# Kernel tuning notes

Measured on AMD Instinct MI355X. Metric: run time of the kernel, lower is better.

## Reference

```python
import jax, jax.numpy as jnp
import numpy as np
from jax import lax

DIM = 384
NH = 8
HD = DIM // NH
M = 16          # num_anchors
B = 16
HH = 64
WW = 64
N = HH * WW
STD = 0.02


def setup_inputs() -> dict:
    key = jax.random.key(0)
    ks = jax.random.split(key, 12)
    rn = lambda k, shape: (jax.random.normal(k, shape, jnp.float32) * STD)
    return {
        "x": jax.random.normal(ks[0], (B, N, DIM), jnp.float32),
        "H": HH,
        "W": WW,
        "saliency_w": rn(ks[1], (DIM, 1)),
        "saliency_b": jnp.zeros((1,), jnp.float32),
        "anchor_seeds": rn(ks[2], (1, M, DIM)),
        "w_q_agg": rn(ks[3], (DIM, DIM)),
        "w_kv_agg": rn(ks[4], (DIM, 2 * DIM)),
        "w_q_self": rn(ks[5], (DIM, DIM)),
        "w_kv_self": rn(ks[6], (DIM, 2 * DIM)),
        "w_q_bcast": rn(ks[7], (DIM, DIM)),
        "w_kv_bcast": rn(ks[8], (DIM, 2 * DIM)),
        "dw_kernel": rn(ks[9], (DIM, 1, 3, 3)),  # depthwise conv, OIHW with I=1
        "w_proj": rn(ks[10], (DIM, DIM)),
    }


def _mhsa(q_in, kv_in, wq, wkv):
    """Multi-head cross attention. q_in: [B,Lq,C], kv_in: [B,Lk,C]."""
    b, lq, c = q_in.shape
    lk = kv_in.shape[1]
    scale = HD ** -0.5
    q = (q_in @ wq).reshape(b, lq, NH, HD)
    kv = (kv_in @ wkv).reshape(b, lk, 2, NH, HD)
    k, v = kv[:, :, 0], kv[:, :, 1]
    attn = jnp.einsum("bqhd,bkhd->bhqk", q, k) * scale
    attn = jax.nn.softmax(attn, axis=-1)
    out = jnp.einsum("bhqk,bkhd->bqhd", attn, v).reshape(b, lq, c)
    return out


def reference(x, H, W, saliency_w, saliency_b, anchor_seeds,
              w_q_agg, w_kv_agg, w_q_self, w_kv_self,
              w_q_bcast, w_kv_bcast, dw_kernel, w_proj):
    b, n, c = x.shape
    # saliency gating
    sal = jax.nn.sigmoid(x @ saliency_w + saliency_b)  # [B,N,1]
    x_sal = x * sal
    # stage 1: anchors aggregate from saliency-gated tokens
    anchors = jnp.broadcast_to(anchor_seeds, (b, M, c))
    anchors = anchors + _mhsa(anchors, x_sal, w_q_agg, w_kv_agg)
    # stage 2: anchor self-attention
    anchors = anchors + _mhsa(anchors, anchors, w_q_self, w_kv_self)
    # stage 3: broadcast anchors back to all tokens
    global_out = _mhsa(x, anchors, w_q_bcast, w_kv_bcast)
    # depthwise 3x3 conv on the 2D token map
    x2d = x.reshape(b, H, W, c).transpose(0, 3, 1, 2)  # NCHW
    local = lax.conv_general_dilated(
        x2d, dw_kernel, window_strides=(1, 1), padding="SAME",
        feature_group_count=c,
        dimension_numbers=("NCHW", "OIHW", "NCHW"))
    local = local.transpose(0, 2, 3, 1).reshape(b, n, c)
    return (global_out + local) @ w_proj
```

## Files before the change

### kernel.cpp

```cpp
#include <hip/hip_runtime.h>
#include <hip/hip_bf16.h>

#define SCALE 0.14433756729740643f

typedef __attribute__((ext_vector_type(8))) short bf16x8;
typedef __attribute__((ext_vector_type(4))) float f32x4;

template <typename T> __device__ inline T cvt_from_f(float v);
template <> __device__ inline float cvt_from_f<float>(float v) { return v; }
template <> __device__ inline __hip_bfloat16 cvt_from_f<__hip_bfloat16>(float v) { return __float2bfloat16(v); }

__device__ inline void gload16(const void* g, void* l) {
  __builtin_amdgcn_global_load_lds((const __attribute__((address_space(1))) void*)g,
                                   (__attribute__((address_space(3))) void*)l, 16, 0, 0);
}

__device__ inline int xcd_flat(int nwg) {
  int flat = (blockIdx.z * gridDim.y + blockIdx.y) * gridDim.x + blockIdx.x;
  int per = nwg >> 3;
  return (flat & 7) * per + (flat >> 3);
}

__global__ __launch_bounds__(256) void prep(const float* __restrict__ x,
                                            const float* __restrict__ wsal,
                                            const float* __restrict__ bsal,
                                            __hip_bfloat16* __restrict__ xb,
                                            float* __restrict__ sal) {
  int wave = threadIdx.x >> 6, lane = threadIdx.x & 63;
  size_t row = (size_t)blockIdx.x * 4 + wave;
  const float* xr = x + row * 384;
  float xs[6];
  float part = 0.f;
#pragma unroll
  for (int j = 0; j < 6; j++) {
    int c = lane + 64 * j;
    xs[j] = xr[c];
    part += xs[j] * wsal[c];
  }
#pragma unroll
  for (int off = 32; off >= 1; off >>= 1) part += __shfl_xor(part, off);
  float s = 1.f / (1.f + __expf(-(part + bsal[0])));
#pragma unroll
  for (int j = 0; j < 6; j++) {
    int c = lane + 64 * j;
    xb[row * 384 + c] = __float2bfloat16(xs[j]);
  }
  if (lane == 0) sal[row] = s;
}

__global__ __launch_bounds__(256) void xtrans(const __hip_bfloat16* __restrict__ xb,
                                              __hip_bfloat16* __restrict__ xbT) {
  __shared__ short t[64][66];
  int n0 = blockIdx.x * 64, c0 = blockIdx.y * 64, b = blockIdx.z;
  int tid = threadIdx.x;
  int r = tid >> 3, c8 = tid & 7;
#pragma unroll
  for (int i = 0; i < 2; i++) {
    int row = r + i * 32;
    bf16x8 v = *(const bf16x8*)(xb + ((size_t)(b * 4096 + n0 + row)) * 384 + c0 + c8 * 8);
    unsigned int* trow = (unsigned int*)&t[row][c8 * 8];
#pragma unroll
    for (int j = 0; j < 4; j++) {
      union { unsigned int u; short s[2]; } p;
      p.s[0] = v[j * 2];
      p.s[1] = v[j * 2 + 1];
      trow[j] = p.u;
    }
  }
  __syncthreads();
#pragma unroll
  for (int i = 0; i < 2; i++) {
    int crow = r + i * 32;
    short tb[8];
#pragma unroll
    for (int j = 0; j < 8; j++) tb[j] = t[c8 * 8 + j][crow];
    *(ulonglong2*)(xbT + ((size_t)b * 384 + c0 + crow) * 4096 + n0 + c8 * 8) = *(ulonglong2*)tb;
  }
}

__global__ void wcast_tv(const float* __restrict__ w, __hip_bfloat16* __restrict__ wt) {
  int idx = blockIdx.x * 256 + threadIdx.x;
  if (idx >= 384 * 384) return;
  int n = idx / 384, k = idx % 384;
  wt[idx] = __float2bfloat16(w[(size_t)k * 768 + 384 + n]);
}

template <int K, typename OT, int BSHIFT>
__global__ __launch_bounds__(256) void gemm_mfma(const __hip_bfloat16* __restrict__ A,
                                                 const __hip_bfloat16* __restrict__ BT,
                                                 OT* __restrict__ out, int Ncols,
                                                 size_t btBatchStride) {
  __shared__ __align__(16) __hip_bfloat16 Asl[128][32];
  __shared__ __align__(16) __hip_bfloat16 Bsl[128][32];
  int nf = xcd_flat(gridDim.x * gridDim.y);
  int bX = nf % gridDim.x, bY = nf / gridDim.x;
  int tid = threadIdx.x;
  int lane = tid & 63;
  int w = tid >> 6;
  int wr = w >> 1, wc = w & 1;
  int fr = lane & 15, fq = lane >> 4;
  int rowBase = bY * 128, colBase = bX * 128;
  const __hip_bfloat16* BTb = BT + (size_t)(rowBase >> BSHIFT) * btBatchStride;

  int r1 = tid >> 2, kc1 = tid & 3;
  int r2 = (tid + 256) >> 2;

  char* aB1 = (char*)Asl + (size_t)(w * 64) * 16;
  char* aB2 = (char*)Asl + (size_t)(256 + w * 64) * 16;
  char* bB1 = (char*)Bsl + (size_t)(w * 64) * 16;
  char* bB2 = (char*)Bsl + (size_t)(256 + w * 64) * 16;

  const __hip_bfloat16* a1 = A + (size_t)(rowBase + r1) * K + kc1 * 8;
  const __hip_bfloat16* a2 = A + (size_t)(rowBase + r2) * K + kc1 * 8;
  const __hip_bfloat16* b1 = BTb + (size_t)(colBase + r1) * K + kc1 * 8;
  const __hip_bfloat16* b2 = BTb + (size_t)(colBase + r2) * K + kc1 * 8;

  f32x4 acc[4][4] = {};

  for (int kk = 0; kk < K; kk += 32) {
    gload16(a1 + kk, aB1);
    gload16(a2 + kk, aB2);
    gload16(b1 + kk, bB1);
    gload16(b2 + kk, bB2);
    __syncthreads();
    bf16x8 af[4], bfv[4];
#pragma unroll
    for (int m = 0; m < 4; m++) af[m] = *(const bf16x8*)&Asl[wr * 64 + m * 16 + fr][fq * 8];
#pragma unroll
    for (int n = 0; n < 4; n++) bfv[n] = *(const bf16x8*)&Bsl[wc * 64 + n * 16 + fr][fq * 8];
#pragma unroll
    for (int m = 0; m < 4; m++)
#pragma unroll
      for (int n = 0; n < 4; n++)
        acc[m][n] = __builtin_amdgcn_mfma_f32_16x16x32_bf16(af[m], bfv[n], acc[m][n], 0, 0, 0);
    __syncthreads();
  }

#pragma unroll
  for (int m = 0; m < 4; m++) {
    int row0 = rowBase + wr * 64 + m * 16 + fq * 4;
#pragma unroll
    for (int n = 0; n < 4; n++) {
      int col = colBase + wc * 64 + n * 16 + fr;
      f32x4 v = acc[m][n];
#pragma unroll
      for (int r = 0; r < 4; r++) out[(size_t)(row0 + r) * Ncols + col] = cvt_from_f<OT>(v[r]);
    }
  }
}

__global__ __launch_bounds__(256) void gemm_logits(const __hip_bfloat16* __restrict__ A,
                                                   const __hip_bfloat16* __restrict__ BT,
                                                   __hip_bfloat16* __restrict__ lgT,
                                                   const float* __restrict__ rowScale) {
  constexpr int K = 384;
  __shared__ __align__(16) __hip_bfloat16 Asl[128][32];
  __shared__ __align__(16) __hip_bfloat16 Bsl[128][32];
  int tid = threadIdx.x;
  int lane = tid & 63;
  int w = tid >> 6;
  int wr = w >> 1, wc = w & 1;
  int fr = lane & 15, fq = lane >> 4;
  int rowBase = blockIdx.x * 128;

  int r1 = tid >> 2, kc1 = tid & 3;
  int r2 = (tid + 256) >> 2;

  char* aB1 = (char*)Asl + (size_t)(w * 64) * 16;
  char* aB2 = (char*)Asl + (size_t)(256 + w * 64) * 16;
  char* bB1 = (char*)Bsl + (size_t)(w * 64) * 16;
  char* bB2 = (char*)Bsl + (size_t)(256 + w * 64) * 16;

  const __hip_bfloat16* a1 = A + (size_t)(rowBase + r1) * K + kc1 * 8;
  const __hip_bfloat16* a2 = A + (size_t)(rowBase + r2) * K + kc1 * 8;
  const __hip_bfloat16* b1 = BT + (size_t)r1 * K + kc1 * 8;
  const __hip_bfloat16* b2 = BT + (size_t)r2 * K + kc1 * 8;

  f32x4 acc[4][4] = {};

  for (int kk = 0; kk < K; kk += 32) {
    gload16(a1 + kk, aB1);
    gload16(a2 + kk, aB2);
    gload16(b1 + kk, bB1);
    gload16(b2 + kk, bB2);
    __syncthreads();
    bf16x8 af[4], bfv[4];
#pragma unroll
    for (int m = 0; m < 4; m++) af[m] = *(const bf16x8*)&Asl[wr * 64 + m * 16 + fr][fq * 8];
#pragma unroll
    for (int n = 0; n < 4; n++) bfv[n] = *(const bf16x8*)&Bsl[wc * 64 + n * 16 + fr][fq * 8];
#pragma unroll
    for (int m = 0; m < 4; m++)
#pragma unroll
      for (int n = 0; n < 4; n++)
        acc[m][n] = __builtin_amdgcn_mfma_f32_16x16x32_bf16(af[m], bfv[n], acc[m][n], 0, 0, 0);
    __syncthreads();
  }

  float sv[4][4];
#pragma unroll
  for (int m = 0; m < 4; m++)
#pragma unroll
    for (int r = 0; r < 4; r++)
      sv[m][r] = rowScale[rowBase + wr * 64 + m * 16 + fq * 4 + r];

#pragma unroll
  for (int m = 0; m < 4; m++) {
    int row0 = rowBase + wr * 64 + m * 16 + fq * 4;
    int bb = row0 >> 12;
    int n0 = row0 & 4095;
#pragma unroll
    for (int n = 0; n < 4; n++) {
      int col = wc * 64 + n * 16 + fr;
      __hip_bfloat16 tb[4];
#pragma unroll
      for (int r = 0; r < 4; r++) tb[r] = __float2bfloat16(acc[m][n][r] * sv[m][r]);
      *(unsigned long long*)(lgT + ((size_t)bb * 128 + col) * 4096 + n0) = *(unsigned long long*)tb;
    }
  }
}

__global__ __launch_bounds__(256) void softmax_rows(const __hip_bfloat16* __restrict__ lgT,
                                                    const float* __restrict__ sal,
                                                    __hip_bfloat16* __restrict__ PT) {
  int g = blockIdx.x;
  const __hip_bfloat16* row = lgT + (size_t)g * 4096;
  int tid = threadIdx.x, wv = tid >> 6, lane = tid & 63;
  __shared__ float redm[4], reds[4];
  float v[16];
  union { ulonglong2 u; __hip_bfloat16 h[8]; } L0, L1;
  L0.u = *(const ulonglong2*)(row + tid * 16);
  L1.u = *(const ulonglong2*)(row + tid * 16 + 8);
#pragma unroll
  for (int i = 0; i < 8; i++) {
    v[i] = __bfloat162float(L0.h[i]);
    v[8 + i] = __bfloat162float(L1.h[i]);
  }
  float mx = v[0];
#pragma unroll
  for (int i = 1; i < 16; i++) mx = fmaxf(mx, v[i]);
#pragma unroll
  for (int off = 1; off < 64; off <<= 1) mx = fmaxf(mx, __shfl_xor(mx, off));
  if (lane == 0) redm[wv] = mx;
  __syncthreads();
  mx = fmaxf(fmaxf(redm[0], redm[1]), fmaxf(redm[2], redm[3]));
  float s = 0.f;
#pragma unroll
  for (int i = 0; i < 16; i++) {
    v[i] = __expf(v[i] - mx);
    s += v[i];
  }
#pragma unroll
  for (int off = 1; off < 64; off <<= 1) s += __shfl_xor(s, off);
  if (lane == 0) reds[wv] = s;
  __syncthreads();
  s = (reds[0] + reds[1]) + (reds[2] + reds[3]);
  float inv = 1.f / s;
  const float* sp = sal + (size_t)(g >> 7) * 4096 + tid * 16;
  float salv[16];
#pragma unroll
  for (int i = 0; i < 4; i++) {
    float4 q = *(const float4*)(sp + i * 4);
    salv[i * 4] = q.x; salv[i * 4 + 1] = q.y; salv[i * 4 + 2] = q.z; salv[i * 4 + 3] = q.w;
  }
  __hip_bfloat16 tb[16];
#pragma unroll
  for (int i = 0; i < 16; i++) tb[i] = __float2bfloat16(v[i] * inv * salv[i]);
  __hip_bfloat16* op = PT + (size_t)g * 4096 + tid * 16;
  *(ulonglong2*)op = *(ulonglong2*)tb;
  *(ulonglong2*)(op + 8) = *(ulonglong2*)(tb + 8);
}

__global__ __launch_bounds__(256) void gemm_pvx(const __hip_bfloat16* __restrict__ PT,
                                                const __hip_bfloat16* __restrict__ xbT,
                                                float* __restrict__ pbuf) {
  __shared__ __align__(16) __hip_bfloat16 Asl[128][32];
  __shared__ __align__(16) __hip_bfloat16 Bsl[128][32];
  int nf = xcd_flat(192);
  int bX = nf % 3, bY = (nf / 3) & 15, kz = nf / 48;
  int tid = threadIdx.x;
  int lane = tid & 63;
  int w = tid >> 6;
  int wr = w >> 1, wc = w & 1;
  int fr = lane & 15, fq = lane >> 4;
  int rowBase = bY * 128, colBase = bX * 128;
  const __hip_bfloat16* BTb = xbT + (size_t)bY * 384 * 4096;

  int r1 = tid >> 2, kc1 = tid & 3;
  int r2 = (tid + 256) >> 2;

  char* aB1 = (char*)Asl + (size_t)(w * 64) * 16;
  char* aB2 = (char*)Asl + (size_t)(256 + w * 64) * 16;
  char* bB1 = (char*)Bsl + (size_t)(w * 64) * 16;
  char* bB2 = (char*)Bsl + (size_t)(256 + w * 64) * 16;

  const __hip_bfloat16* a1 = PT + (size_t)(rowBase + r1) * 4096 + kz * 1024 + kc1 * 8;
  const __hip_bfloat16* a2 = PT + (size_t)(rowBase + r2) * 4096 + kz * 1024 + kc1 * 8;
  const __hip_bfloat16* b1 = BTb + (size_t)(colBase + r1) * 4096 + kz * 1024 + kc1 * 8;
  const __hip_bfloat16* b2 = BTb + (size_t)(colBase + r2) * 4096 + kz * 1024 + kc1 * 8;

  f32x4 acc[4][4] = {};

  for (int kk = 0; kk < 1024; kk += 32) {
    gload16(a1 + kk, aB1);
    gload16(a2 + kk, aB2);
    gload16(b1 + kk, bB1);
    gload16(b2 + kk, bB2);
    __syncthreads();
    bf16x8 af[4], bfv[4];
#pragma unroll
    for (int m = 0; m < 4; m++) af[m] = *(const bf16x8*)&Asl[wr * 64 + m * 16 + fr][fq * 8];
#pragma unroll
    for (int n = 0; n < 4; n++) bfv[n] = *(const bf16x8*)&Bsl[wc * 64 + n * 16 + fr][fq * 8];
#pragma unroll
    for (int m = 0; m < 4; m++)
#pragma unroll
      for (int n = 0; n < 4; n++)
        acc[m][n] = __builtin_amdgcn_mfma_f32_16x16x32_bf16(af[m], bfv[n], acc[m][n], 0, 0, 0);
    __syncthreads();
  }

  float* outz = pbuf + (size_t)kz * 786432;
#pragma unroll
  for (int m = 0; m < 4; m++) {
    int row0 = rowBase + wr * 64 + m * 16 + fq * 4;
#pragma unroll
    for (int n = 0; n < 4; n++) {
      int col = colBase + wc * 64 + n * 16 + fr;
      f32x4 v = acc[m][n];
#pragma unroll
      for (int r = 0; r < 4; r++) outz[(size_t)(row0 + r) * 384 + col] = v[r];
    }
  }
}

__global__ __launch_bounds__(256) void reduce_z(const float* __restrict__ pbuf,
                                                __hip_bfloat16* __restrict__ pvx) {
  int i4 = (blockIdx.x * 256 + threadIdx.x) * 4;
  float4 s = *(const float4*)(pbuf + i4);
#pragma unroll
  for (int z = 1; z < 4; z++) {
    float4 t = *(const float4*)(pbuf + (size_t)z * 786432 + i4);
    s.x += t.x; s.y += t.y; s.z += t.z; s.w += t.w;
  }
  __hip_bfloat16 tb[4] = {__float2bfloat16(s.x), __float2bfloat16(s.y),
                          __float2bfloat16(s.z), __float2bfloat16(s.w)};
  *(unsigned long long*)(pvx + i4) = *(unsigned long long*)tb;
}

__global__ void anch_fix(const float* __restrict__ outF, const float* __restrict__ seeds,
                         float* __restrict__ anch1) {
  int idx = blockIdx.x * 256 + threadIdx.x;
  int b = idx / 6144;
  int rem = idx - b * 6144;
  int m = rem / 384, c = rem - m * 384;
  int h = c / 48;
  anch1[idx] = seeds[rem] + outF[((size_t)b * 128 + h * 16 + m) * 384 + c];
}

__global__ void fill_wl(const float* __restrict__ wkv, const float* __restrict__ qseed,
                        __hip_bfloat16* __restrict__ wvlT) {
  int idx = blockIdx.x * 256 + threadIdx.x;
  int hm = idx / 384, ci = idx - hm * 384;
  int h = hm >> 4, m = hm & 15;
  const float* wp = wkv + (size_t)ci * 768 + h * 48;
  const float* qp = qseed + m * 384 + h * 48;
  float acc = 0.f;
#pragma unroll
  for (int d = 0; d < 48; d++) acc += wp[d] * qp[d];
  wvlT[384 * 384 + idx] = __float2bfloat16(acc);
}

__global__ __launch_bounds__(256) void wtrans(const float* __restrict__ wproj,
                                              __hip_bfloat16* __restrict__ bt2) {
  __shared__ float t[64][65];
  int kt = blockIdx.x * 64, ct = blockIdx.y * 64;
  int tid = threadIdx.x;
  int c = tid & 63, r4 = tid >> 6;
#pragma unroll
  for (int i = 0; i < 16; i++) {
    int r = i * 4 + r4;
    t[r][c] = wproj[(size_t)(kt + r) * 384 + ct + c];
  }
  __syncthreads();
  __hip_bfloat16 vals[16];
#pragma unroll
  for (int i = 0; i < 16; i++) vals[i] = __float2bfloat16(t[c][i * 4 + r4]);
  for (int b = blockIdx.z * 4; b < blockIdx.z * 4 + 4; b++) {
    __hip_bfloat16* dst = bt2 + (size_t)b * 196608;
#pragma unroll
    for (int i = 0; i < 16; i++) {
      int rr = i * 4 + r4;
      dst[(size_t)(ct + rr) * 512 + kt + c] = vals[i];
    }
  }
}

__global__ __launch_bounds__(256) void fill_fold(const float* __restrict__ wq,
                                                 const float* __restrict__ wproj,
                                                 const float* __restrict__ kvb,
                                                 __hip_bfloat16* __restrict__ wpbT,
                                                 __hip_bfloat16* __restrict__ bt2) {
  int b = blockIdx.y;
  int tid = threadIdx.x;
  __shared__ float stage[16][48];
  __shared__ __hip_bfloat16 obuf[16][264];
  if (blockIdx.x < 8) {
    int h = blockIdx.x;
    for (int idx = tid; idx < 768; idx += 256) {
      int m = idx / 48, d = idx % 48;
      stage[m][d] = kvb[(size_t)(b * 16 + m) * 768 + h * 48 + d];
    }
    __syncthreads();
    for (int kbase = 0; kbase < 384; kbase += 256) {
      int chunk = (kbase == 0) ? 256 : 128;
      if (tid < chunk) {
        int k = kbase + tid;
        const float4* wp = (const float4*)(wq + (size_t)k * 384 + h * 48);
        float acc[16] = {};
#pragma unroll
        for (int dq = 0; dq < 12; dq++) {
          float4 wv = wp[dq];
#pragma unroll
          for (int m = 0; m < 16; m++)
            acc[m] += stage[m][dq * 4] * wv.x + stage[m][dq * 4 + 1] * wv.y +
                      stage[m][dq * 4 + 2] * wv.z + stage[m][dq * 4 + 3] * wv.w;
        }
#pragma unroll
        for (int m = 0; m < 16; m++) obuf[m][tid] = __float2bfloat16(acc[m]);
      }
      __syncthreads();
      for (int widx = tid; widx < 16 * chunk; widx += 256) {
        int m = widx / chunk, kk = widx - m * chunk;
        wpbT[(size_t)b * 49152 + (size_t)(h * 16 + m) * 384 + kbase + kk] = obuf[m][kk];
      }
      __syncthreads();
    }
  } else {
    int h = blockIdx.x - 8;
    for (int idx = tid; idx < 768; idx += 256) {
      int m = idx / 48, d = idx % 48;
      stage[m][d] = kvb[(size_t)(b * 16 + m) * 768 + 384 + h * 48 + d];
    }
    __syncthreads();
    for (int cp = tid; cp < 384; cp += 256) {
      float acc[16] = {};
      for (int d = 0; d < 48; d++) {
        float wv = wproj[(size_t)(h * 48 + d) * 384 + cp];
#pragma unroll
        for (int m = 0; m < 16; m++) acc[m] += stage[m][d] * wv;
      }
      __hip_bfloat16 tb[16];
#pragma unroll
      for (int m = 0; m < 16; m++) tb[m] = __float2bfloat16(acc[m]);
      __hip_bfloat16* dst = bt2 + (size_t)b * 196608 + (size_t)cp * 512 + 384 + h * 16;
      *(ulonglong2*)dst = *(ulonglong2*)tb;
      *(ulonglong2*)(dst + 8) = *(ulonglong2*)(tb + 8);
    }
  }
}

__global__ __launch_bounds__(256) void pgemm(const __hip_bfloat16* __restrict__ A,
                                             const __hip_bfloat16* __restrict__ wpbT,
                                             __hip_bfloat16* __restrict__ A2) {
  constexpr int K = 384;
  __shared__ __align__(16) __hip_bfloat16 Asl[128][32];
  __shared__ __align__(16) __hip_bfloat16 Bsl[128][32];
  int tid = threadIdx.x;
  int lane = tid & 63;
  int w = tid >> 6;
  int wr = w >> 1, wc = w & 1;
  int fr = lane & 15, fq = lane >> 4;
  int rowBase = blockIdx.y * 128;
  const __hip_bfloat16* BTb = wpbT + (size_t)(rowBase >> 12) * (128 * 384);

  int r1 = tid >> 2, kc1 = tid & 3;
  int r2 = (tid + 256) >> 2;

  char* aB1 = (char*)Asl + (size_t)(w * 64) * 16;
  char* aB2 = (char*)Asl + (size_t)(256 + w * 64) * 16;
  char* bB1 = (char*)Bsl + (size_t)(w * 64) * 16;
  char* bB2 = (char*)Bsl + (size_t)(256 + w * 64) * 16;

  const __hip_bfloat16* a1 = A + (size_t)(rowBase + r1) * K + kc1 * 8;
  const __hip_bfloat16* a2 = A + (size_t)(rowBase + r2) * K + kc1 * 8;
  const __hip_bfloat16* b1 = BTb + (size_t)r1 * K + kc1 * 8;
  const __hip_bfloat16* b2 = BTb + (size_t)r2 * K + kc1 * 8;

  f32x4 acc[4][4] = {};

  for (int kk = 0; kk < K; kk += 32) {
    gload16(a1 + kk, aB1);
    gload16(a2 + kk, aB2);
    gload16(b1 + kk, bB1);
    gload16(b2 + kk, bB2);
    __syncthreads();
    bf16x8 af[4], bfv[4];
#pragma unroll
    for (int m = 0; m < 4; m++) af[m] = *(const bf16x8*)&Asl[wr * 64 + m * 16 + fr][fq * 8];
#pragma unroll
    for (int n = 0; n < 4; n++) bfv[n] = *(const bf16x8*)&Bsl[wc * 64 + n * 16 + fr][fq * 8];
#pragma unroll
    for (int m = 0; m < 4; m++)
#pragma unroll
      for (int n = 0; n < 4; n++)
        acc[m][n] = __builtin_amdgcn_mfma_f32_16x16x32_bf16(af[m], bfv[n], acc[m][n], 0, 0, 0);
    __syncthreads();
  }

#pragma unroll
  for (int m = 0; m < 4; m++) {
    int row0 = rowBase + wr * 64 + m * 16 + fq * 4;
#pragma unroll
    for (int n = 0; n < 4; n++) {
      int col = wc * 64 + n * 16 + fr;
      f32x4 v = acc[m][n];
      f32x4 mx = v;
#pragma unroll
      for (int off = 1; off < 16; off <<= 1)
#pragma unroll
        for (int r = 0; r < 4; r++) mx[r] = fmaxf(mx[r], __shfl_xor(mx[r], off));
      f32x4 e;
#pragma unroll
      for (int r = 0; r < 4; r++) e[r] = __expf(v[r] - mx[r]);
      f32x4 s = e;
#pragma unroll
      for (int off = 1; off < 16; off <<= 1)
#pragma unroll
        for (int r = 0; r < 4; r++) s[r] += __shfl_xor(s[r], off);
#pragma unroll
      for (int r = 0; r < 4; r++)
        A2[(size_t)(row0 + r) * 512 + 384 + col] = __float2bfloat16(e[r] / s[r]);
    }
  }
}

__global__ __launch_bounds__(256) void dwconv3(const __hip_bfloat16* __restrict__ xb,
                                               const float* __restrict__ dwk,
                                               __hip_bfloat16* __restrict__ A2) {
  int b = blockIdx.y;
  int y = blockIdx.x;
  int w = threadIdx.x >> 6, lane = threadIdx.x & 63;
  int c0 = lane * 6;
  int x0 = w * 16;
  float kw[9][6];
#pragma unroll
  for (int ki = 0; ki < 9; ki++)
#pragma unroll
    for (int i = 0; i < 6; i++) kw[ki][i] = dwk[(c0 + i) * 9 + ki];

  const __hip_bfloat16* base = xb + ((size_t)(b * 4096 + y * 64)) * 384 + c0;
  bool yv[3];
#pragma unroll
  for (int t = 0; t < 3; t++) {
    int yy = y + t - 1;
    yv[t] = (yy >= 0 && yy < 64);
  }

  float colL[3][6], colC[3][6], colR[3][6];
  auto loadcol = [&](float (&dst)[3][6], int x) {
#pragma unroll
    for (int t = 0; t < 3; t++) {
      if (yv[t]) {
        const __hip_bfloat16* p = base + ((size_t)(t - 1) * 64 + x) * 384;
#pragma unroll
        for (int i = 0; i < 6; i++) dst[t][i] = __bfloat162float(p[i]);
      } else {
#pragma unroll
        for (int i = 0; i < 6; i++) dst[t][i] = 0.f;
      }
    }
  };

  if (x0 == 0) {
#pragma unroll
    for (int t = 0; t < 3; t++)
#pragma unroll
      for (int i = 0; i < 6; i++) colL[t][i] = 0.f;
  } else {
    loadcol(colL, x0 - 1);
  }
  loadcol(colC, x0);

  for (int step = 0; step < 16; step++) {
    int x = x0 + step;
    if (x + 1 < 64) {
      loadcol(colR, x + 1);
    } else {
#pragma unroll
      for (int t = 0; t < 3; t++)
#pragma unroll
        for (int i = 0; i < 6; i++) colR[t][i] = 0.f;
    }
    float acc[6];
#pragma unroll
    for (int i = 0; i < 6; i++) {
      float a = 0.f;
#pragma unroll
      for (int t = 0; t < 3; t++)
        a += colL[t][i] * kw[t * 3 + 0][i] + colC[t][i] * kw[t * 3 + 1][i] +
             colR[t][i] * kw[t * 3 + 2][i];
      acc[i] = a;
    }
    __hip_bfloat16 tb[6];
#pragma unroll
    for (int i = 0; i < 6; i++) tb[i] = __float2bfloat16(acc[i]);
    __hip_bfloat16* gp = A2 + ((size_t)(b * 4096 + y * 64 + x)) * 512 + c0;
    *(unsigned int*)(gp) = *(unsigned int*)(tb);
    *(unsigned int*)(gp + 2) = *(unsigned int*)(tb + 2);
    *(unsigned int*)(gp + 4) = *(unsigned int*)(tb + 4);
#pragma unroll
    for (int t = 0; t < 3; t++)
#pragma unroll
      for (int i = 0; i < 6; i++) {
        colL[t][i] = colC[t][i];
        colC[t][i] = colR[t][i];
      }
  }
}

__global__ __launch_bounds__(256) void anchor_proj2(const float* __restrict__ A,
                                                    const float* __restrict__ W,
                                                    float* __restrict__ out, int wstride,
                                                    int scaleCols) {
  int cs = blockIdx.x * 16;
  int b = blockIdx.y;
  __shared__ float a1[16][385];
  int tid = threadIdx.x;
  for (int idx = tid; idx < 6144; idx += 256) a1[idx / 384][idx % 384] = A[b * 6144 + idx];
  __syncthreads();
  int m = tid >> 4, cc = tid & 15;
  int col = cs + cc;
  const float* wp = W + col;
  float acc0 = 0.f, acc1 = 0.f, acc2 = 0.f, acc3 = 0.f;
#pragma unroll 4
  for (int k = 0; k < 384; k += 4) {
    acc0 += a1[m][k] * wp[(size_t)k * wstride];
    acc1 += a1[m][k + 1] * wp[(size_t)(k + 1) * wstride];
    acc2 += a1[m][k + 2] * wp[(size_t)(k + 2) * wstride];
    acc3 += a1[m][k + 3] * wp[(size_t)(k + 3) * wstride];
  }
  float acc = (acc0 + acc1) + (acc2 + acc3);
  if (col < scaleCols) acc *= SCALE;
  out[((size_t)b * 16 + m) * wstride + col] = acc;
}

__global__ __launch_bounds__(256) void anchor_proj_qkv(const float* __restrict__ A,
                                                       const float* __restrict__ Wq,
                                                       const float* __restrict__ Wkv,
                                                       float* __restrict__ q_out,
                                                       float* __restrict__ kv_out) {
  bool isQ = blockIdx.x < 24;
  int bx = isQ ? blockIdx.x : blockIdx.x - 24;
  const float* W = isQ ? Wq : Wkv;
  float* outp = isQ ? q_out : kv_out;
  int wstride = isQ ? 384 : 768;
  float scale = isQ ? SCALE : 1.f;
  int cs = bx * 16;
  int b = blockIdx.y;
  __shared__ float a1[16][385];
  int tid = threadIdx.x;
  for (int idx = tid; idx < 6144; idx += 256) a1[idx / 384][idx % 384] = A[b * 6144 + idx];
  __syncthreads();
  int m = tid >> 4, cc = tid & 15;
  int col = cs + cc;
  const float* wp = W + col;
  float acc0 = 0.f, acc1 = 0.f, acc2 = 0.f, acc3 = 0.f;
#pragma unroll 4
  for (int k = 0; k < 384; k += 4) {
    acc0 += a1[m][k] * wp[(size_t)k * wstride];
    acc1 += a1[m][k + 1] * wp[(size_t)(k + 1) * wstride];
    acc2 += a1[m][k + 2] * wp[(size_t)(k + 2) * wstride];
    acc3 += a1[m][k + 3] * wp[(size_t)(k + 3) * wstride];
  }
  float acc = ((acc0 + acc1) + (acc2 + acc3)) * scale;
  outp[((size_t)b * 16 + m) * wstride + col] = acc;
}

__global__ void self_attn(const float* __restrict__ qsf, const float* __restrict__ kvs,
                          const float* __restrict__ anch1, float* __restrict__ anch2) {
  int h = blockIdx.x & 7, b = blockIdx.x >> 3;
  __shared__ float qs[16][48], ks[16][48], vs[16][48], p[16][17];
  int tid = threadIdx.x;
  for (int idx = tid; idx < 768; idx += 256) {
    int m = idx / 48, d = idx % 48;
    qs[m][d] = qsf[(b * 16 + m) * 384 + h * 48 + d];
    ks[m][d] = kvs[(b * 16 + m) * 768 + h * 48 + d];
    vs[m][d] = kvs[(b * 16 + m) * 768 + 384 + h * 48 + d];
  }
  __syncthreads();
  {
    int mq = tid >> 4, mk = tid & 15;
    float acc = 0.f;
    for (int d = 0; d < 48; d++) acc += qs[mq][d] * ks[mk][d];
    p[mq][mk] = acc;
  }
  __syncthreads();
  if (tid < 16) {
    float mx = -1e30f;
    for (int mk = 0; mk < 16; mk++) mx = fmaxf(mx, p[tid][mk]);
    float sum = 0.f;
    for (int mk = 0; mk < 16; mk++) {
      float e = __expf(p[tid][mk] - mx);
      p[tid][mk] = e;
      sum += e;
    }
    float inv = 1.f / sum;
    for (int mk = 0; mk < 16; mk++) p[tid][mk] *= inv;
  }
  __syncthreads();
  for (int idx = tid; idx < 768; idx += 256) {
    int m = idx / 48, d = idx % 48;
    float acc = 0.f;
    for (int mk = 0; mk < 16; mk++) acc += p[m][mk] * vs[mk][d];
    int c = h * 48 + d;
    anch2[(b * 16 + m) * 384 + c] = anch1[(b * 16 + m) * 384 + c] + acc;
  }
}

extern "C" void kernel_launch(void* const* d_in, const int* in_sizes, int n_in,
                              void* d_out, int out_size, void* d_ws, size_t ws_size,
                              hipStream_t stream) {
  (void)in_sizes; (void)n_in; (void)out_size; (void)ws_size;
  const float* x = (const float*)d_in[0];
  const float* wsal = (const float*)d_in[3];
  const float* bsal = (const float*)d_in[4];
  const float* seeds = (const float*)d_in[5];
  const float* w_q_agg = (const float*)d_in[6];
  const float* w_kv_agg = (const float*)d_in[7];
  const float* w_q_self = (const float*)d_in[8];
  const float* w_kv_self = (const float*)d_in[9];
  const float* w_q_bcast = (const float*)d_in[10];
  const float* w_kv_bcast = (const float*)d_in[11];
  const float* dwk = (const float*)d_in[12];
  const float* w_proj = (const float*)d_in[13];
  float* out = (float*)d_out;

  char* ws = (char*)d_ws;
  size_t off = 0;
  auto take = [&](size_t bytes) -> void* {
    void* p = ws + off;
    off += (bytes + 255) & ~(size_t)255;
    return p;
  };
  __hip_bfloat16* xb = (__hip_bfloat16*)take(50331648);
  __hip_bfloat16* xbT = (__hip_bfloat16*)take(50331648);
  char* R = (char*)take(67108864);
  __hip_bfloat16* PT = (__hip_bfloat16*)take(16777216);
  __hip_bfloat16* pvx = (__hip_bfloat16*)take(1572864);
  float* outF = (float*)take(3145728);
  float* qseed = (float*)take(24576);
  float* sal = (float*)take(262144);
  float* anch1 = (float*)take(393216);
  float* anch2 = (float*)take(393216);
  float* q_self = (float*)take(393216);
  float* kv_self = (float*)take(786432);
  float* kv_b = (float*)take(786432);
  __hip_bfloat16* wvlT = (__hip_bfloat16*)take(393216);
  __hip_bfloat16* wpbT = (__hip_bfloat16*)take(1572864);
  __hip_bfloat16* bt2 = (__hip_bfloat16*)take(6291456);
  __hip_bfloat16* logitsT = (__hip_bfloat16*)R;
  float* pbuf = (float*)R;
  __hip_bfloat16* A2 = (__hip_bfloat16*)R;

  prep<<<16384, 256, 0, stream>>>(x, wsal, bsal, xb, sal);
  xtrans<<<dim3(64, 6, 16), 256, 0, stream>>>(xb, xbT);
  anchor_proj2<<<dim3(24, 1), 256, 0, stream>>>(seeds, w_q_agg, qseed, 384, 384);
  wcast_tv<<<576, 256, 0, stream>>>(w_kv_agg, wvlT);
  fill_wl<<<192, 256, 0, stream>>>(w_kv_agg, qseed, wvlT);
  wtrans<<<dim3(6, 6, 4), 256, 0, stream>>>(w_proj, bt2);
  gemm_logits<<<512, 256, 0, stream>>>(xb, wvlT + 384 * 384, logitsT, sal);
  softmax_rows<<<2048, 256, 0, stream>>>(logitsT, sal, PT);
  gemm_pvx<<<dim3(3, 16, 4), 256, 0, stream>>>(PT, xbT, pbuf);
  reduce_z<<<768, 256, 0, stream>>>(pbuf, pvx);
  gemm_mfma<384, float, 12><<<dim3(3, 16), 256, 0, stream>>>(pvx, wvlT, outF, 384, 0);
  anch_fix<<<384, 256, 0, stream>>>(outF, seeds, anch1);
  anchor_proj_qkv<<<dim3(72, 16), 256, 0, stream>>>(anch1, w_q_self, w_kv_self, q_self, kv_self);
  self_attn<<<128, 256, 0, stream>>>(q_self, kv_self, anch1, anch2);
  anchor_proj2<<<dim3(48, 16), 256, 0, stream>>>(anch2, w_kv_bcast, kv_b, 768, 384);
  fill_fold<<<dim3(16, 16), 256, 0, stream>>>(w_q_bcast, w_proj, kv_b, wpbT, bt2);
  pgemm<<<dim3(1, 512), 256, 0, stream>>>(xb, wpbT, A2);
  dwconv3<<<dim3(64, 16), 256, 0, stream>>>(xb, dwk, A2);
  gemm_mfma<512, float, 12><<<dim3(3, 512), 256, 0, stream>>>(A2, bt2, out, 384, (size_t)384 * 512);
}
```

Baseline: 352.7 us.

## Fuse prep with transpose and use a BK=64 swizzled final GEMM

Merges the saliency/bf16-cast prep kernel with the x transpose kernel, so each block keeps 64 rows in LDS and writes both xb and xbT without re-reading xb from global memory. It also replaces the final output GEMM with a dedicated kernel that uses a K-tile of 64 and an XOR-swizzled LDS layout, halving the K-loop iterations and barriers and cutting LDS bank conflicts. The fused prep kernel uses about 50KB of LDS and launches only 1024 blocks, which may lower occupancy.

```diff
diff --git a/kernel.cpp b/kernel.cpp
--- a/kernel.cpp
+++ b/kernel.cpp
@@ -21,60 +21,55 @@
   return (flat & 7) * per + (flat >> 3);
 }
 
-__global__ __launch_bounds__(256) void prep(const float* __restrict__ x,
-                                            const float* __restrict__ wsal,
-                                            const float* __restrict__ bsal,
-                                            __hip_bfloat16* __restrict__ xb,
-                                            float* __restrict__ sal) {
-  int wave = threadIdx.x >> 6, lane = threadIdx.x & 63;
-  size_t row = (size_t)blockIdx.x * 4 + wave;
-  const float* xr = x + row * 384;
-  float xs[6];
-  float part = 0.f;
-#pragma unroll
-  for (int j = 0; j < 6; j++) {
-    int c = lane + 64 * j;
-    xs[j] = xr[c];
-    part += xs[j] * wsal[c];
-  }
-#pragma unroll
-  for (int off = 32; off >= 1; off >>= 1) part += __shfl_xor(part, off);
-  float s = 1.f / (1.f + __expf(-(part + bsal[0])));
-#pragma unroll
-  for (int j = 0; j < 6; j++) {
-    int c = lane + 64 * j;
-    xb[row * 384 + c] = __float2bfloat16(xs[j]);
-  }
-  if (lane == 0) sal[row] = s;
-}
-
-__global__ __launch_bounds__(256) void xtrans(const __hip_bfloat16* __restrict__ xb,
-                                              __hip_bfloat16* __restrict__ xbT) {
-  __shared__ short t[64][66];
-  int n0 = blockIdx.x * 64, c0 = blockIdx.y * 64, b = blockIdx.z;
-  int tid = threadIdx.x;
-  int r = tid >> 3, c8 = tid & 7;
-#pragma unroll
-  for (int i = 0; i < 2; i++) {
-    int row = r + i * 32;
-    bf16x8 v = *(const bf16x8*)(xb + ((size_t)(b * 4096 + n0 + row)) * 384 + c0 + c8 * 8);
-    unsigned int* trow = (unsigned int*)&t[row][c8 * 8];
-#pragma unroll
-    for (int j = 0; j < 4; j++) {
-      union { unsigned int u; short s[2]; } p;
-      p.s[0] = v[j * 2];
-      p.s[1] = v[j * 2 + 1];
-      trow[j] = p.u;
-    }
+__global__ __launch_bounds__(256) void prep_trans(const float* __restrict__ x,
+                                                  const float* __restrict__ wsal,
+                                                  const float* __restrict__ bsal,
+                                                  __hip_bfloat16* __restrict__ xb,
+                                                  __hip_bfloat16* __restrict__ xbT,
+                                                  float* __restrict__ sal) {
+  __shared__ short ts[6][64][66];
+  int wv = threadIdx.x >> 6, lane = threadIdx.x & 63;
+  size_t rowBase = (size_t)blockIdx.x * 64;
+  float bs = bsal[0];
+  for (int it = 0; it < 16; it++) {
+    int r = it * 4 + wv;
+    size_t row = rowBase + r;
+    const float* xr = x + row * 384;
+    float xs[6];
+    float part = 0.f;
+#pragma unroll
+    for (int j = 0; j < 6; j++) {
+      int c = lane + 64 * j;
+      xs[j] = xr[c];
+      part += xs[j] * wsal[c];
+    }
+#pragma unroll
+    for (int off = 32; off >= 1; off >>= 1) part += __shfl_xor(part, off);
+    float s = 1.f / (1.f + __expf(-(part + bs)));
+#pragma unroll
+    for (int j = 0; j < 6; j++) {
+      int c = lane + 64 * j;
+      __hip_bfloat16 hv = __float2bfloat16(xs[j]);
+      xb[row * 384 + c] = hv;
+      ts[j][r][lane] = *(short*)&hv;
+    }
+    if (lane == 0) sal[row] = s;
   }
   __syncthreads();
-#pragma unroll
-  for (int i = 0; i < 2; i++) {
-    int crow = r + i * 32;
-    short tb[8];
-#pragma unroll
-    for (int j = 0; j < 8; j++) tb[j] = t[c8 * 8 + j][crow];
-    *(ulonglong2*)(xbT + ((size_t)b * 384 + c0 + crow) * 4096 + n0 + c8 * 8) = *(ulonglong2*)tb;
+  int b = blockIdx.x >> 6;
+  int n0 = (int)(rowBase & 4095);
+  int r2 = threadIdx.x >> 3, c8 = threadIdx.x & 7;
+#pragma unroll
+  for (int jt = 0; jt < 6; jt++) {
+#pragma unroll
+    for (int i = 0; i < 2; i++) {
+      int crow = r2 + i * 32;
+      short tb[8];
+#pragma unroll
+      for (int kk = 0; kk < 8; kk++) tb[kk] = ts[jt][c8 * 8 + kk][crow];
+      *(ulonglong2*)(xbT + ((size_t)b * 384 + jt * 64 + crow) * 4096 + n0 + c8 * 8) =
+          *(ulonglong2*)tb;
+    }
   }
 }
 
@@ -145,6 +140,81 @@
       f32x4 v = acc[m][n];
 #pragma unroll
       for (int r = 0; r < 4; r++) out[(size_t)(row0 + r) * Ncols + col] = cvt_from_f<OT>(v[r]);
+    }
+  }
+}
+
+__global__ __launch_bounds__(256) void gemm_out(const __hip_bfloat16* __restrict__ A,
+                                                const __hip_bfloat16* __restrict__ BT,
+                                                float* __restrict__ out) {
+  __shared__ __align__(16) __hip_bfloat16 Asl[128][64];
+  __shared__ __align__(16) __hip_bfloat16 Bsl[128][64];
+  int nf = xcd_flat(1536);
+  int bX = nf % 3, bY = nf / 3;
+  int tid = threadIdx.x;
+  int lane = tid & 63;
+  int w = tid >> 6;
+  int wr = w >> 1, wc = w & 1;
+  int fr = lane & 15, fq = lane >> 4;
+  int rowBase = bY * 128, colBase = bX * 128;
+  const __hip_bfloat16* BTb = BT + (size_t)(rowBase >> 12) * (384 * 512);
+
+  int r0 = tid >> 3, jc = tid & 7;
+  int kc = jc ^ (r0 & 7);
+  char* aB[4];
+  char* bB[4];
+  const __hip_bfloat16* a_src[4];
+  const __hip_bfloat16* b_src[4];
+#pragma unroll
+  for (int i = 0; i < 4; i++) {
+    aB[i] = (char*)Asl + (size_t)(i * 256 + w * 64) * 16;
+    bB[i] = (char*)Bsl + (size_t)(i * 256 + w * 64) * 16;
+    a_src[i] = A + (size_t)(rowBase + r0 + i * 32) * 512 + kc * 8;
+    b_src[i] = BTb + (size_t)(colBase + r0 + i * 32) * 512 + kc * 8;
+  }
+
+  f32x4 acc[4][4] = {};
+
+  for (int kk = 0; kk < 512; kk += 64) {
+#pragma unroll
+    for (int i = 0; i < 4; i++) {
+      gload16(a_src[i] + kk, aB[i]);
+      gload16(b_src[i] + kk, bB[i]);
+    }
+    __syncthreads();
+#pragma unroll
+    for (int half = 0; half < 2; half++) {
+      bf16x8 af[4], bfv[4];
+#pragma unroll
+      for (int m = 0; m < 4; m++) {
+        int row = wr * 64 + m * 16 + fr;
+        af[m] = *(const bf16x8*)((char*)Asl + (size_t)row * 128 +
+                                 (((fq + 4 * half) ^ (row & 7)) << 4));
+      }
+#pragma unroll
+      for (int n = 0; n < 4; n++) {
+        int row = wc * 64 + n * 16 + fr;
+        bfv[n] = *(const bf16x8*)((char*)Bsl + (size_t)row * 128 +
+                                  (((fq + 4 * half) ^ (row & 7)) << 4));
+      }
+#pragma unroll
+      for (int m = 0; m < 4; m++)
+#pragma unroll
+        for (int n = 0; n < 4; n++)
+          acc[m][n] = __builtin_amdgcn_mfma_f32_16x16x32_bf16(af[m], bfv[n], acc[m][n], 0, 0, 0);
+    }
+    __syncthreads();
+  }
+
+#pragma unroll
+  for (int m = 0; m < 4; m++) {
+    int row0 = rowBase + wr * 64 + m * 16 + fq * 4;
+#pragma unroll
+    for (int n = 0; n < 4; n++) {
+      int col = colBase + wc * 64 + n * 16 + fr;
+      f32x4 v = acc[m][n];
+#pragma unroll
+      for (int r = 0; r < 4; r++) out[(size_t)(row0 + r) * 384 + col] = v[r];
     }
   }
 }
@@ -763,8 +833,7 @@
   float* pbuf = (float*)R;
   __hip_bfloat16* A2 = (__hip_bfloat16*)R;
 
-  prep<<<16384, 256, 0, stream>>>(x, wsal, bsal, xb, sal);
-  xtrans<<<dim3(64, 6, 16), 256, 0, stream>>>(xb, xbT);
+  prep_trans<<<1024, 256, 0, stream>>>(x, wsal, bsal, xb, xbT, sal);
   anchor_proj2<<<dim3(24, 1), 256, 0, stream>>>(seeds, w_q_agg, qseed, 384, 384);
   wcast_tv<<<576, 256, 0, stream>>>(w_kv_agg, wvlT);
   fill_wl<<<192, 256, 0, stream>>>(w_kv_agg, qseed, wvlT);
@@ -781,5 +850,5 @@
   fill_fold<<<dim3(16, 16), 256, 0, stream>>>(w_q_bcast, w_proj, kv_b, wpbT, bt2);
   pgemm<<<dim3(1, 512), 256, 0, stream>>>(xb, wpbT, A2);
   dwconv3<<<dim3(64, 16), 256, 0, stream>>>(xb, dwk, A2);
-  gemm_mfma<512, float, 12><<<dim3(3, 512), 256, 0, stream>>>(A2, bt2, out, 384, (size_t)384 * 512);
-}
+  gemm_out<<<dim3(3, 512), 256, 0, stream>>>(A2, bt2, out);
+}
```

Result: no change. 347.1 us (-1.6%).
